# Kernel optimization log

Measured on AMD Instinct MI355X. Metric: run time of the kernel, lower is better.

## Reference

```python
import jax, jax.numpy as jnp
import numpy as np

B, I, O, T, L, K, PAD = 16, 256, 256, 512, 8192, 7, 3
EPS = 1e-8


def setup_inputs() -> dict:
    key = jax.random.key(0)
    ks = jax.random.split(key, 7)
    bx = jax.random.normal(ks[0], (B, I, L), dtype=jnp.float32)
    t = jax.random.normal(ks[1], (B, T), dtype=jnp.float32)
    # depthwise conv weight: torch Conv1d(groups=I) weight is (I, 1, K)
    conv_w = jax.random.normal(ks[2], (I, 1, K), dtype=jnp.float32) * (1.0 / np.sqrt(K))
    # 1x1 proj: torch Conv1d weight (O, I, 1) -> store as (O, I)
    proj_w = jax.random.normal(ks[3], (O, I), dtype=jnp.float32) * (1.0 / np.sqrt(I))
    proj_b = jax.random.normal(ks[4], (O,), dtype=jnp.float32) * 0.01
    # Linear(t_dim -> in_dim)
    mod_w = jax.random.normal(ks[5], (I, T), dtype=jnp.float32) * (1.0 / np.sqrt(T))
    mod_b = jax.random.normal(ks[6], (I,), dtype=jnp.float32) * 0.01
    return {"bx": bx, "t": t, "conv_w": conv_w, "proj_w": proj_w,
            "proj_b": proj_b, "mod_w": mod_w, "mod_b": mod_b}


def reference(bx, t, conv_w, proj_w, proj_b, mod_w, mod_b):
    # modulation: (B, I)
    mod = t @ mod_w.T + mod_b
    # per-sample modulated 1x1 weights: (B, O, I)
    bw = proj_w[None, :, :] * (mod[:, None, :] + 1.0)
    # demodulation (L2 over input dim, kernel dim is size 1)
    demod = jax.lax.rsqrt(jnp.sum(bw * bw, axis=2) + EPS)  # (B, O)
    bw = bw * demod[:, :, None]
    # depthwise conv over length, 'same' padding (kernel 7, pad 3)
    xc = jax.lax.conv_general_dilated(
        bx, conv_w,
        window_strides=(1,), padding=[(PAD, PAD)],
        dimension_numbers=('NCH', 'OIH', 'NCH'),
        feature_group_count=I)  # (B, I, L)
    # per-sample grouped 1x1 conv == batched matmul
    out = jnp.einsum('boi,bil->bol', bw, xc) + proj_b[None, :, None]
    return out
```

## Files before the change

kernel.cpp:

```cpp
#include <hip/hip_runtime.h>
#include <hip/hip_bf16.h>

#define B_ 16
#define I_ 256
#define O_ 256
#define T_ 512
#define L_ 8192
#define K_ 7
#define PAD_ 3
#define BN 64
#define LDK 264

typedef unsigned short u16;
typedef unsigned int u32;
typedef __attribute__((ext_vector_type(8))) short short8;
typedef __attribute__((ext_vector_type(4))) float f32x4;

__device__ inline u16 f2bf(float f) {
    union { float f; u32 u; } v; v.f = f;
    u32 r = v.u + 0x7FFF + ((v.u >> 16) & 1);
    return (u16)(r >> 16);
}

__global__ void mod_kernel(const float* __restrict__ t, const float* __restrict__ mod_w,
                           const float* __restrict__ mod_b, float* __restrict__ mod) {
    int g = blockIdx.x, b = blockIdx.y;
    int lane = threadIdx.x & 63, wv = threadIdx.x >> 6;
    const float* tb = t + b * T_;
    #pragma unroll
    for (int q = 0; q < 4; ++q) {
        int i = g * 16 + wv * 4 + q;
        const float* wr = mod_w + (size_t)i * T_;
        float s = 0.f;
        #pragma unroll
        for (int u = 0; u < 8; ++u) s += wr[lane + u * 64] * tb[lane + u * 64];
        #pragma unroll
        for (int d = 32; d; d >>= 1) s += __shfl_down(s, d);
        if (lane == 0) mod[b * I_ + i] = s + mod_b[i];
    }
}

__global__ void wmod_kernel(const float* __restrict__ proj_w, const float* __restrict__ mod,
                            u16* __restrict__ Wb) {
    int og = blockIdx.x, b = blockIdx.y;
    int lane = threadIdx.x & 63, wv = threadIdx.x >> 6;
    const float* mrow = mod + b * I_;
    #pragma unroll
    for (int q = 0; q < 4; ++q) {
        int o = og * 16 + wv * 4 + q;
        const float* pw = proj_w + (size_t)o * I_;
        float4 pv = *(const float4*)(pw + lane * 4);
        float4 mv = *(const float4*)(mrow + lane * 4);
        float v0 = pv.x * (mv.x + 1.f);
        float v1 = pv.y * (mv.y + 1.f);
        float v2 = pv.z * (mv.z + 1.f);
        float v3 = pv.w * (mv.w + 1.f);
        float ss = v0*v0 + v1*v1 + v2*v2 + v3*v3;
        #pragma unroll
        for (int d = 32; d; d >>= 1) ss += __shfl_xor(ss, d);
        float dem = rsqrtf(ss + 1e-8f);
        u32 lo = (u32)f2bf(v0 * dem) | ((u32)f2bf(v1 * dem) << 16);
        u32 hi = (u32)f2bf(v2 * dem) | ((u32)f2bf(v3 * dem) << 16);
        *(uint2*)(Wb + (size_t)(b * O_ + o) * I_ + lane * 4) = make_uint2(lo, hi);
    }
}

__global__ __launch_bounds__(256) void main_kernel(
    const float* __restrict__ bx, const float* __restrict__ conv_w,
    const u16* __restrict__ Wb, const float* __restrict__ proj_b,
    float* __restrict__ out)
{
    __shared__ __align__(16) u16 Xs[BN * LDK];

    const int tile = blockIdx.x;
    const int b = blockIdx.y;
    const int l0 = tile * BN;
    const int tid = threadIdx.x;
    const int lane = tid & 63;
    const int wv = tid >> 6;
    const int mlane = lane & 15;
    const int quad = lane >> 4;

    const int rq = tid >> 2;
    const int lq = tid & 3;
    const int i0 = rq * 4;
    const float* bxr = bx + (size_t)b * I_ * L_;
    const bool interior = (l0 >= 4) && (l0 + 72 <= L_);

    float wr[4][K_];
    #pragma unroll
    for (int di = 0; di < 4; ++di)
        #pragma unroll
        for (int j = 0; j < K_; ++j)
            wr[di][j] = conv_w[(i0 + di) * K_ + j];

    for (int it = 0; it < 4; ++it) {
        const int lb = it * 16 + lq * 4;
        u16 hv[4][4];
        #pragma unroll
        for (int di = 0; di < 4; ++di) {
            const float* row = bxr + (size_t)(i0 + di) * L_ + l0;
            float x[12];
            if (interior) {
                const float4* rp = (const float4*)(row + lb - 4);
                float4 w0 = rp[0], w1 = rp[1], w2 = rp[2];
                x[0]=w0.x; x[1]=w0.y; x[2]=w0.z; x[3]=w0.w;
                x[4]=w1.x; x[5]=w1.y; x[6]=w1.z; x[7]=w1.w;
                x[8]=w2.x; x[9]=w2.y; x[10]=w2.z; x[11]=w2.w;
            } else {
                #pragma unroll
                for (int w = 0; w < 12; ++w) {
                    int p = l0 + lb - 4 + w;
                    x[w] = (p >= 0 && p < L_) ? row[lb - 4 + w] : 0.f;
                }
            }
            #pragma unroll
            for (int dl = 0; dl < 4; ++dl) {
                float a = 0.f;
                #pragma unroll
                for (int j = 0; j < K_; ++j) a += wr[di][j] * x[dl + 1 + j];
                hv[dl][di] = f2bf(a);
            }
        }
        #pragma unroll
        for (int dl = 0; dl < 4; ++dl) {
            int n = lb + dl;
            u32 lo = (u32)hv[dl][0] | ((u32)hv[dl][1] << 16);
            u32 hi = (u32)hv[dl][2] | ((u32)hv[dl][3] << 16);
            *(uint2*)(&Xs[n * LDK + i0]) = make_uint2(lo, hi);
        }
    }
    __syncthreads();

    f32x4 acc[4][4];
    #pragma unroll
    for (int r = 0; r < 4; ++r)
        #pragma unroll
        for (int c = 0; c < 4; ++c)
            acc[r][c] = (f32x4){0.f, 0.f, 0.f, 0.f};

    const u16* Wrow = Wb + (size_t)(b * O_ + wv * 64 + mlane) * I_;

    for (int kb = 0; kb < 8; ++kb) {
        const int koff = kb * 32 + quad * 8;
        short8 a[4], bbf[4];
        #pragma unroll
        for (int r = 0; r < 4; ++r)
            a[r] = *(const short8*)(Wrow + r * 16 * I_ + koff);
        #pragma unroll
        for (int c = 0; c < 4; ++c)
            bbf[c] = *(const short8*)(&Xs[(c * 16 + mlane) * LDK + koff]);
        #pragma unroll
        for (int r = 0; r < 4; ++r)
            #pragma unroll
            for (int c = 0; c < 4; ++c)
                acc[r][c] = __builtin_amdgcn_mfma_f32_16x16x32_bf16(a[r], bbf[c], acc[r][c], 0, 0, 0);
    }

    float* outb = out + (size_t)b * O_ * L_;
    #pragma unroll
    for (int r = 0; r < 4; ++r) {
        const int obase = wv * 64 + r * 16 + quad * 4;
        #pragma unroll
        for (int p = 0; p < 4; ++p) {
            const int o = obase + p;
            const float bias = proj_b[o];
            float* orow = outb + (size_t)o * L_ + l0 + mlane;
            #pragma unroll
            for (int c = 0; c < 4; ++c)
                orow[c * 16] = acc[r][c][p] + bias;
        }
    }
}

extern "C" void kernel_launch(void* const* d_in, const int* in_sizes, int n_in,
                              void* d_out, int out_size, void* d_ws, size_t ws_size,
                              hipStream_t stream) {
    const float* bx     = (const float*)d_in[0];
    const float* t      = (const float*)d_in[1];
    const float* conv_w = (const float*)d_in[2];
    const float* proj_w = (const float*)d_in[3];
    const float* proj_b = (const float*)d_in[4];
    const float* mod_w  = (const float*)d_in[5];
    const float* mod_b  = (const float*)d_in[6];
    float* out = (float*)d_out;

    float* mod = (float*)d_ws;
    u16*   Wb  = (u16*)((char*)d_ws + 16384);

    mod_kernel<<<dim3(16, 16), 256, 0, stream>>>(t, mod_w, mod_b, mod);
    wmod_kernel<<<dim3(16, 16), 256, 0, stream>>>(proj_w, mod, Wb);
    main_kernel<<<dim3(128, 16), 256, 0, stream>>>(bx, conv_w, Wb, proj_b, out);
}
```

Before: 317.1 us.

## Warp-specialize main kernel into conv producers and MFMA consumers with double-buffered LDS

Splits each 512-thread block into four producer waves that compute the depthwise conv into a double-buffered LDS tile and four consumer waves that run the bf16 MFMA projection on the previous tile. Each block now processes four consecutive length tiles, pipelining conv of tile n+1 with the GEMM of tile n. This aims to overlap global loads and conv ALU work with matrix work, at the cost of fewer blocks, doubled LDS usage and reduced occupancy.

```diff
diff --git a/kernel.cpp b/kernel.cpp
--- a/kernel.cpp
+++ b/kernel.cpp
@@ -9,6 +9,7 @@
 #define K_ 7
 #define PAD_ 3
 #define BN 64
+#define NT 4
 #define LDK 264
 
 typedef unsigned short u16;
@@ -65,110 +66,169 @@
     }
 }
 
-__global__ __launch_bounds__(256) void main_kernel(
+__global__ __launch_bounds__(512, 4) void main_kernel(
     const float* __restrict__ bx, const float* __restrict__ conv_w,
     const u16* __restrict__ Wb, const float* __restrict__ proj_b,
     float* __restrict__ out)
 {
-    __shared__ __align__(16) u16 Xs[BN * LDK];
-
-    const int tile = blockIdx.x;
+    __shared__ __align__(16) u16 Xs[2][BN * LDK];
+
     const int b = blockIdx.y;
-    const int l0 = tile * BN;
+    const int tg0 = blockIdx.x * NT;
     const int tid = threadIdx.x;
-    const int lane = tid & 63;
     const int wv = tid >> 6;
-    const int mlane = lane & 15;
-    const int quad = lane >> 4;
-
-    const int rq = tid >> 2;
-    const int lq = tid & 3;
-    const int i0 = rq * 4;
-    const float* bxr = bx + (size_t)b * I_ * L_;
-    const bool interior = (l0 >= 4) && (l0 + 72 <= L_);
-
-    float wr[4][K_];
-    #pragma unroll
-    for (int di = 0; di < 4; ++di)
-        #pragma unroll
-        for (int j = 0; j < K_; ++j)
-            wr[di][j] = conv_w[(i0 + di) * K_ + j];
-
-    for (int it = 0; it < 4; ++it) {
-        const int lb = it * 16 + lq * 4;
-        u16 hv[4][4];
-        #pragma unroll
-        for (int di = 0; di < 4; ++di) {
-            const float* row = bxr + (size_t)(i0 + di) * L_ + l0;
-            float x[12];
-            if (interior) {
-                const float4* rp = (const float4*)(row + lb - 4);
-                float4 w0 = rp[0], w1 = rp[1], w2 = rp[2];
-                x[0]=w0.x; x[1]=w0.y; x[2]=w0.z; x[3]=w0.w;
-                x[4]=w1.x; x[5]=w1.y; x[6]=w1.z; x[7]=w1.w;
-                x[8]=w2.x; x[9]=w2.y; x[10]=w2.z; x[11]=w2.w;
-            } else {
-                #pragma unroll
-                for (int w = 0; w < 12; ++w) {
-                    int p = l0 + lb - 4 + w;
-                    x[w] = (p >= 0 && p < L_) ? row[lb - 4 + w] : 0.f;
-                }
-            }
+    const bool producer = (wv < 4);
+
+    if (producer) {
+        const int rq = tid >> 2;
+        const int lq = tid & 3;
+        const int i0 = rq * 4;
+        const float* bxr = bx + (size_t)b * I_ * L_;
+
+        float wr[4][K_];
+        #pragma unroll
+        for (int di = 0; di < 4; ++di)
             #pragma unroll
-            for (int dl = 0; dl < 4; ++dl) {
-                float a = 0.f;
-                #pragma unroll
-                for (int j = 0; j < K_; ++j) a += wr[di][j] * x[dl + 1 + j];
-                hv[dl][di] = f2bf(a);
-            }
+            for (int j = 0; j < K_; ++j)
+                wr[di][j] = conv_w[(i0 + di) * K_ + j];
+
+        for (int tt = 0; tt < NT; ++tt) {
+            const int l0 = (tg0 + tt) * BN;
+            u16* xsb = Xs[tt & 1];
+            const bool interior = (l0 >= 4) && (l0 + 72 <= L_);
+
+            for (int it = 0; it < 4; ++it) {
+                const int lb = it * 16 + lq * 4;
+                u16 hv[4][4];
+                #pragma unroll
+                for (int di = 0; di < 4; ++di) {
+                    const float* row = bxr + (size_t)(i0 + di) * L_ + l0;
+                    float x[12];
+                    if (interior) {
+                        const float4* rp = (const float4*)(row + lb - 4);
+                        float4 w0 = rp[0], w1 = rp[1], w2 = rp[2];
+                        x[0]=w0.x; x[1]=w0.y; x[2]=w0.z; x[3]=w0.w;
+                        x[4]=w1.x; x[5]=w1.y; x[6]=w1.z; x[7]=w1.w;
+                        x[8]=w2.x; x[9]=w2.y; x[10]=w2.z; x[11]=w2.w;
+                    } else {
+                        #pragma unroll
+                        for (int w = 0; w < 12; ++w) {
+                            int p = l0 + lb - 4 + w;
+                            x[w] = (p >= 0 && p < L_) ? row[lb - 4 + w] : 0.f;
+                        }
+                    }
+                    #pragma unroll
+                    for (int dl = 0; dl < 4; ++dl) {
+                        float a = 0.f;
+                        #pragma unroll
+                        for (int j = 0; j < K_; ++j) a += wr[di][j] * x[dl + 1 + j];
+                        hv[dl][di] = f2bf(a);
+                    }
+                }
+                #pragma unroll
+                for (int dl = 0; dl < 4; ++dl) {
+                    int n = lb + dl;
+                    u32 lo = (u32)hv[dl][0] | ((u32)hv[dl][1] << 16);
+                    u32 hi = (u32)hv[dl][2] | ((u32)hv[dl][3] << 16);
+                    *(uint2*)(&xsb[n * LDK + i0]) = make_uint2(lo, hi);
+                }
+            }
+            __syncthreads();
         }
-        #pragma unroll
-        for (int dl = 0; dl < 4; ++dl) {
-            int n = lb + dl;
-            u32 lo = (u32)hv[dl][0] | ((u32)hv[dl][1] << 16);
-            u32 hi = (u32)hv[dl][2] | ((u32)hv[dl][3] << 16);
-            *(uint2*)(&Xs[n * LDK + i0]) = make_uint2(lo, hi);
+    } else {
+        const int ctid = tid - 256;
+        const int lane = ctid & 63;
+        const int wg = ctid >> 6;
+        const int mlane = lane & 15;
+        const int quad = lane >> 4;
+        const u16* Wrow = Wb + (size_t)(b * O_ + wg * 64 + mlane) * I_;
+        float* outb = out + (size_t)b * O_ * L_;
+
+        for (int tt = 0; tt < NT; ++tt) {
+            if (tt > 0) {
+                const int l0 = (tg0 + tt - 1) * BN;
+                const u16* xsb = Xs[(tt - 1) & 1];
+
+                f32x4 acc[4][4];
+                #pragma unroll
+                for (int r = 0; r < 4; ++r)
+                    #pragma unroll
+                    for (int c = 0; c < 4; ++c)
+                        acc[r][c] = (f32x4){0.f, 0.f, 0.f, 0.f};
+
+                for (int kb = 0; kb < 8; ++kb) {
+                    const int koff = kb * 32 + quad * 8;
+                    short8 a[4], bbf[4];
+                    #pragma unroll
+                    for (int r = 0; r < 4; ++r)
+                        a[r] = *(const short8*)(Wrow + r * 16 * I_ + koff);
+                    #pragma unroll
+                    for (int c = 0; c < 4; ++c)
+                        bbf[c] = *(const short8*)(&xsb[(c * 16 + mlane) * LDK + koff]);
+                    #pragma unroll
+                    for (int r = 0; r < 4; ++r)
+                        #pragma unroll
+                        for (int c = 0; c < 4; ++c)
+                            acc[r][c] = __builtin_amdgcn_mfma_f32_16x16x32_bf16(a[r], bbf[c], acc[r][c], 0, 0, 0);
+                }
+
+                #pragma unroll
+                for (int r = 0; r < 4; ++r) {
+                    const int obase = wg * 64 + r * 16 + quad * 4;
+                    #pragma unroll
+                    for (int p = 0; p < 4; ++p) {
+                        const int o = obase + p;
+                        const float bias = proj_b[o];
+                        float* orow = outb + (size_t)o * L_ + l0 + mlane;
+                        #pragma unroll
+                        for (int c = 0; c < 4; ++c)
+                            orow[c * 16] = acc[r][c][p] + bias;
+                    }
+                }
+            }
+            __syncthreads();
         }
-    }
-    __syncthreads();
-
-    f32x4 acc[4][4];
-    #pragma unroll
-    for (int r = 0; r < 4; ++r)
-        #pragma unroll
-        for (int c = 0; c < 4; ++c)
-            acc[r][c] = (f32x4){0.f, 0.f, 0.f, 0.f};
-
-    const u16* Wrow = Wb + (size_t)(b * O_ + wv * 64 + mlane) * I_;
-
-    for (int kb = 0; kb < 8; ++kb) {
-        const int koff = kb * 32 + quad * 8;
-        short8 a[4], bbf[4];
-        #pragma unroll
-        for (int r = 0; r < 4; ++r)
-            a[r] = *(const short8*)(Wrow + r * 16 * I_ + koff);
-        #pragma unroll
-        for (int c = 0; c < 4; ++c)
-            bbf[c] = *(const short8*)(&Xs[(c * 16 + mlane) * LDK + koff]);
-        #pragma unroll
-        for (int r = 0; r < 4; ++r)
+
+        {
+            const int l0 = (tg0 + NT - 1) * BN;
+            const u16* xsb = Xs[(NT - 1) & 1];
+
+            f32x4 acc[4][4];
             #pragma unroll
-            for (int c = 0; c < 4; ++c)
-                acc[r][c] = __builtin_amdgcn_mfma_f32_16x16x32_bf16(a[r], bbf[c], acc[r][c], 0, 0, 0);
-    }
-
-    float* outb = out + (size_t)b * O_ * L_;
-    #pragma unroll
-    for (int r = 0; r < 4; ++r) {
-        const int obase = wv * 64 + r * 16 + quad * 4;
-        #pragma unroll
-        for (int p = 0; p < 4; ++p) {
-            const int o = obase + p;
-            const float bias = proj_b[o];
-            float* orow = outb + (size_t)o * L_ + l0 + mlane;
+            for (int r = 0; r < 4; ++r)
+                #pragma unroll
+                for (int c = 0; c < 4; ++c)
+                    acc[r][c] = (f32x4){0.f, 0.f, 0.f, 0.f};
+
+            for (int kb = 0; kb < 8; ++kb) {
+                const int koff = kb * 32 + quad * 8;
+                short8 a[4], bbf[4];
+                #pragma unroll
+                for (int r = 0; r < 4; ++r)
+                    a[r] = *(const short8*)(Wrow + r * 16 * I_ + koff);
+                #pragma unroll
+                for (int c = 0; c < 4; ++c)
+                    bbf[c] = *(const short8*)(&xsb[(c * 16 + mlane) * LDK + koff]);
+                #pragma unroll
+                for (int r = 0; r < 4; ++r)
+                    #pragma unroll
+                    for (int c = 0; c < 4; ++c)
+                        acc[r][c] = __builtin_amdgcn_mfma_f32_16x16x32_bf16(a[r], bbf[c], acc[r][c], 0, 0, 0);
+            }
+
             #pragma unroll
-            for (int c = 0; c < 4; ++c)
-                orow[c * 16] = acc[r][c][p] + bias;
+            for (int r = 0; r < 4; ++r) {
+                const int obase = wg * 64 + r * 16 + quad * 4;
+                #pragma unroll
+                for (int p = 0; p < 4; ++p) {
+                    const int o = obase + p;
+                    const float bias = proj_b[o];
+                    float* orow = outb + (size_t)o * L_ + l0 + mlane;
+                    #pragma unroll
+                    for (int c = 0; c < 4; ++c)
+                        orow[c * 16] = acc[r][c][p] + bias;
+                }
+            }
         }
     }
 }
@@ -190,5 +250,5 @@
 
     mod_kernel<<<dim3(16, 16), 256, 0, stream>>>(t, mod_w, mod_b, mod);
     wmod_kernel<<<dim3(16, 16), 256, 0, stream>>>(proj_w, mod, Wb);
-    main_kernel<<<dim3(128, 16), 256, 0, stream>>>(bx, conv_w, Wb, proj_b, out);
-}
+    main_kernel<<<dim3(32, 16), 512, 0, stream>>>(bx, conv_w, Wb, proj_b, out);
+}
```

After: 383.7 us. 21.0% more time.

## Stage input halo tile in LDS via global_load_lds before depthwise conv

Applied to the files above, without the earlier changes.

Replaces the per-thread float4 global loads plus halo re-reads with a two-pass scheme. Each pass stages 128 channels × 77 columns of the input into shared memory using direct global-to-LDS loads, zero-fills edge padding for the first and last tiles, and then computes the 7-tap conv per channel from LDS. This removes redundant halo fetches and the interior/boundary branching. In exchange it adds about 40KB of LDS, which limits occupancy, uses 4-byte scalar DMA loads, and adds extra barriers. It also writes Xs with scattered 2-byte stores that may cause bank conflicts.

```diff
diff --git a/kernel.cpp b/kernel.cpp
--- a/kernel.cpp
+++ b/kernel.cpp
@@ -9,7 +9,10 @@
 #define K_ 7
 #define PAD_ 3
 #define BN 64
+#define NTILE 128
 #define LDK 264
+#define XFS 77
+#define XFN 9984
 
 typedef unsigned short u16;
 typedef unsigned int u32;
@@ -70,6 +73,7 @@
     const u16* __restrict__ Wb, const float* __restrict__ proj_b,
     float* __restrict__ out)
 {
+    __shared__ __align__(16) float Xf[XFN];
     __shared__ __align__(16) u16 Xs[BN * LDK];
 
     const int tile = blockIdx.x;
@@ -80,57 +84,64 @@
     const int wv = tid >> 6;
     const int mlane = lane & 15;
     const int quad = lane >> 4;
-
-    const int rq = tid >> 2;
-    const int lq = tid & 3;
-    const int i0 = rq * 4;
     const float* bxr = bx + (size_t)b * I_ * L_;
-    const bool interior = (l0 >= 4) && (l0 + 72 <= L_);
-
-    float wr[4][K_];
-    #pragma unroll
-    for (int di = 0; di < 4; ++di)
-        #pragma unroll
-        for (int j = 0; j < K_; ++j)
-            wr[di][j] = conv_w[(i0 + di) * K_ + j];
-
-    for (int it = 0; it < 4; ++it) {
-        const int lb = it * 16 + lq * 4;
-        u16 hv[4][4];
-        #pragma unroll
-        for (int di = 0; di < 4; ++di) {
-            const float* row = bxr + (size_t)(i0 + di) * L_ + l0;
-            float x[12];
-            if (interior) {
-                const float4* rp = (const float4*)(row + lb - 4);
-                float4 w0 = rp[0], w1 = rp[1], w2 = rp[2];
-                x[0]=w0.x; x[1]=w0.y; x[2]=w0.z; x[3]=w0.w;
-                x[4]=w1.x; x[5]=w1.y; x[6]=w1.z; x[7]=w1.w;
-                x[8]=w2.x; x[9]=w2.y; x[10]=w2.z; x[11]=w2.w;
-            } else {
+
+    const int ch_init = tid / XFS;
+    const int col_init = tid - ch_init * XFS;
+
+    for (int ck = 0; ck < 2; ++ck) {
+        const int ci0 = ck << 7;
+
+        {
+            int ch = ch_init, col = col_init;
+            #pragma unroll
+            for (int k = 0; k < 39; ++k) {
+                int chc = ch < 127 ? ch : 127;
+                int p = l0 - 4 + col;
+                p = p < 0 ? 0 : (p > L_ - 1 ? L_ - 1 : p);
+                const float* gp = bxr + (size_t)(ci0 + chc) * L_ + p;
+                __builtin_amdgcn_global_load_lds(
+                    (const __attribute__((address_space(1))) u32*)gp,
+                    (__attribute__((address_space(3))) u32*)&Xf[k * 256 + tid], 4, 0, 0);
+                ch += 3; col += 25;
+                if (col >= XFS) { col -= XFS; ch += 1; }
+            }
+        }
+        __syncthreads();
+
+        if (tile == 0) {
+            for (int z = tid; z < 128 * 4; z += 256)
+                Xf[(z >> 2) * XFS + (z & 3)] = 0.f;
+            __syncthreads();
+        } else if (tile == NTILE - 1) {
+            for (int z = tid; z < 128 * 9; z += 256) {
+                int r = z / 9;
+                Xf[r * XFS + 68 + (z - r * 9)] = 0.f;
+            }
+            __syncthreads();
+        }
+
+        {
+            const int chl = tid & 127;
+            const int a = (tid >> 7) << 5;
+            const int ig = ci0 + chl;
+            float w[K_];
+            #pragma unroll
+            for (int j = 0; j < K_; ++j) w[j] = conv_w[ig * K_ + j];
+            const float* xr = &Xf[chl * XFS + a];
+            float x[39];
+            #pragma unroll
+            for (int m = 1; m <= 38; ++m) x[m] = xr[m];
+            #pragma unroll
+            for (int n = 0; n < 32; ++n) {
+                float s = 0.f;
                 #pragma unroll
-                for (int w = 0; w < 12; ++w) {
-                    int p = l0 + lb - 4 + w;
-                    x[w] = (p >= 0 && p < L_) ? row[lb - 4 + w] : 0.f;
-                }
+                for (int j = 0; j < K_; ++j) s += w[j] * x[n + 1 + j];
+                Xs[(a + n) * LDK + ig] = f2bf(s);
             }
-            #pragma unroll
-            for (int dl = 0; dl < 4; ++dl) {
-                float a = 0.f;
-                #pragma unroll
-                for (int j = 0; j < K_; ++j) a += wr[di][j] * x[dl + 1 + j];
-                hv[dl][di] = f2bf(a);
-            }
-        }
-        #pragma unroll
-        for (int dl = 0; dl < 4; ++dl) {
-            int n = lb + dl;
-            u32 lo = (u32)hv[dl][0] | ((u32)hv[dl][1] << 16);
-            u32 hi = (u32)hv[dl][2] | ((u32)hv[dl][3] << 16);
-            *(uint2*)(&Xs[n * LDK + i0]) = make_uint2(lo, hi);
-        }
-    }
-    __syncthreads();
+        }
+        __syncthreads();
+    }
 
     f32x4 acc[4][4];
     #pragma unroll
```

Result: faster. 303.7 us (-4.2%).

## Make main kernel persistent over tiles with async global-to-LDS prefetch of input

Applied to the files above, without the earlier changes.

Each block now handles 8 consecutive length tiles of one batch with 512 threads. The next tile's raw input window is prefetched into LDS with global_load_lds so the load overlaps the current tile's MFMA and store work. The modulated weight fragments and bias are loaded into registers once per block rather than once per tile. The depthwise conv is now computed per channel from LDS with clamped loads and explicit zeroing at the edges. In exchange the grid shrinks to 256 blocks, LDS use grows to about 107 KB per block, and register pressure rises.

```diff
diff --git a/kernel.cpp b/kernel.cpp
--- a/kernel.cpp
+++ b/kernel.cpp
@@ -9,7 +9,11 @@
 #define K_ 7
 #define PAD_ 3
 #define BN 64
+#define NT 8
+#define GROUPS 16
 #define LDK 264
+#define XFS 71
+#define XFN 18432
 
 typedef unsigned short u16;
 typedef unsigned int u32;
@@ -65,110 +69,121 @@
     }
 }
 
-__global__ __launch_bounds__(256) void main_kernel(
+#define STAGE(L0T) do { \
+    int ch = ch0, col = col0; \
+    _Pragma("unroll") \
+    for (int k = 0; k < 36; ++k) { \
+        int chc = ch < 255 ? ch : 255; \
+        int p = (L0T) - 4 + col; \
+        p = p < 0 ? 0 : (p > L_ - 1 ? L_ - 1 : p); \
+        const float* gp = bxr + (size_t)chc * L_ + p; \
+        __builtin_amdgcn_global_load_lds( \
+            (const __attribute__((address_space(1))) u32*)gp, \
+            (__attribute__((address_space(3))) u32*)&Xf[k * 512 + tid], 4, 0, 0); \
+        ch += 7; col += 15; \
+        if (col >= XFS) { col -= XFS; ch += 1; } \
+    } } while (0)
+
+__global__ __launch_bounds__(512, 2) void main_kernel(
     const float* __restrict__ bx, const float* __restrict__ conv_w,
     const u16* __restrict__ Wb, const float* __restrict__ proj_b,
     float* __restrict__ out)
 {
+    __shared__ __align__(16) float Xf[XFN];
     __shared__ __align__(16) u16 Xs[BN * LDK];
 
-    const int tile = blockIdx.x;
-    const int b = blockIdx.y;
-    const int l0 = tile * BN;
+    const int id = blockIdx.x;
+    const int b = id & 15;
+    const int group = id >> 4;
     const int tid = threadIdx.x;
     const int lane = tid & 63;
     const int wv = tid >> 6;
     const int mlane = lane & 15;
     const int quad = lane >> 4;
-
-    const int rq = tid >> 2;
-    const int lq = tid & 3;
-    const int i0 = rq * 4;
     const float* bxr = bx + (size_t)b * I_ * L_;
-    const bool interior = (l0 >= 4) && (l0 + 72 <= L_);
-
-    float wr[4][K_];
-    #pragma unroll
-    for (int di = 0; di < 4; ++di)
-        #pragma unroll
-        for (int j = 0; j < K_; ++j)
-            wr[di][j] = conv_w[(i0 + di) * K_ + j];
-
-    for (int it = 0; it < 4; ++it) {
-        const int lb = it * 16 + lq * 4;
-        u16 hv[4][4];
-        #pragma unroll
-        for (int di = 0; di < 4; ++di) {
-            const float* row = bxr + (size_t)(i0 + di) * L_ + l0;
-            float x[12];
-            if (interior) {
-                const float4* rp = (const float4*)(row + lb - 4);
-                float4 w0 = rp[0], w1 = rp[1], w2 = rp[2];
-                x[0]=w0.x; x[1]=w0.y; x[2]=w0.z; x[3]=w0.w;
-                x[4]=w1.x; x[5]=w1.y; x[6]=w1.z; x[7]=w1.w;
-                x[8]=w2.x; x[9]=w2.y; x[10]=w2.z; x[11]=w2.w;
-            } else {
+    float* outb = out + (size_t)b * O_ * L_;
+
+    const int cch = tid & 255;
+    const int half = tid >> 8;
+    const int ch0 = tid / XFS;
+    const int col0 = tid - ch0 * XFS;
+
+    float w[K_];
+    #pragma unroll
+    for (int j = 0; j < K_; ++j) w[j] = conv_w[cch * K_ + j];
+
+    short8 aF[2][8];
+    const u16* Wrow = Wb + (size_t)(b * O_ + wv * 32 + mlane) * I_;
+    #pragma unroll
+    for (int r = 0; r < 2; ++r)
+        #pragma unroll
+        for (int kb = 0; kb < 8; ++kb)
+            aF[r][kb] = *(const short8*)(Wrow + r * 16 * I_ + kb * 32 + quad * 8);
+
+    float bias[2][4];
+    #pragma unroll
+    for (int r = 0; r < 2; ++r)
+        #pragma unroll
+        for (int p = 0; p < 4; ++p)
+            bias[r][p] = proj_b[wv * 32 + r * 16 + quad * 4 + p];
+
+    STAGE(group * NT * BN);
+
+    for (int t = 0; t < NT; ++t) {
+        const int tile = group * NT + t;
+        const int l0 = tile * BN;
+        __syncthreads();
+
+        {
+            const float* xr = &Xf[cch * XFS + half * 32];
+            float x[38];
+            #pragma unroll
+            for (int m = 0; m < 38; ++m) x[m] = xr[1 + m];
+            if (tile == 0 && half == 0)       { x[0] = 0.f; x[1] = 0.f; x[2] = 0.f; }
+            if (tile == 127 && half == 1)     { x[35] = 0.f; x[36] = 0.f; x[37] = 0.f; }
+            #pragma unroll
+            for (int n = 0; n < 32; ++n) {
+                float s = 0.f;
                 #pragma unroll
-                for (int w = 0; w < 12; ++w) {
-                    int p = l0 + lb - 4 + w;
-                    x[w] = (p >= 0 && p < L_) ? row[lb - 4 + w] : 0.f;
-                }
-            }
-            #pragma unroll
-            for (int dl = 0; dl < 4; ++dl) {
-                float a = 0.f;
-                #pragma unroll
-                for (int j = 0; j < K_; ++j) a += wr[di][j] * x[dl + 1 + j];
-                hv[dl][di] = f2bf(a);
+                for (int j = 0; j < K_; ++j) s += w[j] * x[n + j];
+                Xs[(half * 32 + n) * LDK + cch] = f2bf(s);
             }
         }
-        #pragma unroll
-        for (int dl = 0; dl < 4; ++dl) {
-            int n = lb + dl;
-            u32 lo = (u32)hv[dl][0] | ((u32)hv[dl][1] << 16);
-            u32 hi = (u32)hv[dl][2] | ((u32)hv[dl][3] << 16);
-            *(uint2*)(&Xs[n * LDK + i0]) = make_uint2(lo, hi);
+        __syncthreads();
+
+        if (t + 1 < NT) STAGE(l0 + BN);
+
+        f32x4 acc[2][4];
+        #pragma unroll
+        for (int r = 0; r < 2; ++r)
+            #pragma unroll
+            for (int c = 0; c < 4; ++c)
+                acc[r][c] = (f32x4){0.f, 0.f, 0.f, 0.f};
+
+        #pragma unroll
+        for (int kb = 0; kb < 8; ++kb) {
+            const int koff = kb * 32 + quad * 8;
+            short8 bbf[4];
+            #pragma unroll
+            for (int c = 0; c < 4; ++c)
+                bbf[c] = *(const short8*)(&Xs[(c * 16 + mlane) * LDK + koff]);
+            #pragma unroll
+            for (int r = 0; r < 2; ++r)
+                #pragma unroll
+                for (int c = 0; c < 4; ++c)
+                    acc[r][c] = __builtin_amdgcn_mfma_f32_16x16x32_bf16(aF[r][kb], bbf[c], acc[r][c], 0, 0, 0);
         }
-    }
-    __syncthreads();
-
-    f32x4 acc[4][4];
-    #pragma unroll
-    for (int r = 0; r < 4; ++r)
-        #pragma unroll
-        for (int c = 0; c < 4; ++c)
-            acc[r][c] = (f32x4){0.f, 0.f, 0.f, 0.f};
-
-    const u16* Wrow = Wb + (size_t)(b * O_ + wv * 64 + mlane) * I_;
-
-    for (int kb = 0; kb < 8; ++kb) {
-        const int koff = kb * 32 + quad * 8;
-        short8 a[4], bbf[4];
-        #pragma unroll
-        for (int r = 0; r < 4; ++r)
-            a[r] = *(const short8*)(Wrow + r * 16 * I_ + koff);
-        #pragma unroll
-        for (int c = 0; c < 4; ++c)
-            bbf[c] = *(const short8*)(&Xs[(c * 16 + mlane) * LDK + koff]);
-        #pragma unroll
-        for (int r = 0; r < 4; ++r)
-            #pragma unroll
-            for (int c = 0; c < 4; ++c)
-                acc[r][c] = __builtin_amdgcn_mfma_f32_16x16x32_bf16(a[r], bbf[c], acc[r][c], 0, 0, 0);
-    }
-
-    float* outb = out + (size_t)b * O_ * L_;
-    #pragma unroll
-    for (int r = 0; r < 4; ++r) {
-        const int obase = wv * 64 + r * 16 + quad * 4;
-        #pragma unroll
-        for (int p = 0; p < 4; ++p) {
-            const int o = obase + p;
-            const float bias = proj_b[o];
-            float* orow = outb + (size_t)o * L_ + l0 + mlane;
-            #pragma unroll
-            for (int c = 0; c < 4; ++c)
-                orow[c * 16] = acc[r][c][p] + bias;
+
+        #pragma unroll
+        for (int r = 0; r < 2; ++r) {
+            const int obase = wv * 32 + r * 16 + quad * 4;
+            #pragma unroll
+            for (int p = 0; p < 4; ++p) {
+                float* orow = outb + (size_t)(obase + p) * L_ + l0 + mlane;
+                #pragma unroll
+                for (int c = 0; c < 4; ++c)
+                    orow[c * 16] = acc[r][c][p] + bias[r][p];
+            }
         }
     }
 }
@@ -190,5 +205,5 @@
 
     mod_kernel<<<dim3(16, 16), 256, 0, stream>>>(t, mod_w, mod_b, mod);
     wmod_kernel<<<dim3(16, 16), 256, 0, stream>>>(proj_w, mod, Wb);
-    main_kernel<<<dim3(128, 16), 256, 0, stream>>>(bx, conv_w, Wb, proj_b, out);
-}
+    main_kernel<<<dim3(GROUPS * 16), 512, 0, stream>>>(bx, conv_w, Wb, proj_b, out);
+}
```

Measured after the change: 271.5 us. 1.17x faster.
